# Kernel tuning notes

Hardware: AMD Instinct MI355X
Metric: run time of the kernel (lower is better)

Reference implementation:

```python
import jax, jax.numpy as jnp
import numpy as np


def setup_inputs() -> dict:
    key = jax.random.key(0)
    ks = jax.random.split(key, 6)
    B, N_in, N_out, D_in, D_out, S = 64, 195, 778, 256, 128, 9
    nnz = 3 * N_out
    x = jax.random.normal(ks[0], (B, N_in, D_in), dtype=jnp.float32)
    # upsample transform: each output vertex receives 3 weighted source verts
    row = jnp.repeat(jnp.arange(N_out, dtype=jnp.int64), 3)
    col = jax.random.randint(ks[1], (nnz,), 0, N_in).astype(jnp.int64)
    value = jax.random.uniform(ks[2], (nnz,), dtype=jnp.float32)
    indices = jax.random.randint(ks[3], (N_out, S), 0, N_out).astype(jnp.int64)
    W = jax.random.normal(ks[4], (D_in * S, D_out), dtype=jnp.float32) * 0.02
    b = jnp.zeros((D_out,), dtype=jnp.float32)
    return {"x": x, "row": row, "col": col, "value": value,
            "indices": indices, "W": W, "b": b}


def reference(x, row, col, value, indices, W, b):
    B, N_in, D = x.shape
    N_out, S = indices.shape
    # Pool: gather source verts, scale by barycentric weight, scatter-add
    msg = x[:, col, :] * value[None, :, None]                # (B, nnz, D)
    pooled = jnp.zeros((B, N_out, D), x.dtype).at[:, row, :].add(msg)
    # SpiralConv: gather spiral neighborhood, flatten, linear
    g = pooled[:, indices.reshape(-1), :].reshape(B, N_out, S * D)
    out = jnp.einsum('bnk,ko->bno', g, W) + b                # (B, N_out, D_out)
    return jax.nn.relu(out)
```

## Files before the change

kernel.cpp:

```cpp
#include <hip/hip_runtime.h>
#include <hip/hip_bf16.h>
#include <stdint.h>

#define N_IN 195
#define N_OUT 778
#define D_IN 256
#define D_OUTC 128
#define NS 9
#define KTOT 2304
#define MM 49792
#define BM 256
#define BK 64
#define NWG 195
#define XE 3194880
#define XCVT_BLOCKS 1560
#define POOL_BLOCKS 6224
#define WT_BLOCKS 1152

using short8  = __attribute__((ext_vector_type(8))) short;
using f32x4   = __attribute__((ext_vector_type(4))) float;

__device__ __forceinline__ void gload16(const void* g, void* l) {
  __builtin_amdgcn_global_load_lds(
      (const __attribute__((address_space(1))) uint32_t*)g,
      (__attribute__((address_space(3))) uint32_t*)l, 16, 0, 0);
}

__device__ __forceinline__ unsigned short f2bf(float f) {
  uint32_t u = __float_as_uint(f);
  return (unsigned short)((u + 0x7FFFu + ((u >> 16) & 1u)) >> 16);
}
__device__ __forceinline__ float bf2f(unsigned short s) {
  return __uint_as_float(((uint32_t)s) << 16);
}

__global__ __launch_bounds__(256) void xcvt_kernel(
    const float* __restrict__ x, unsigned short* __restrict__ xh) {
  int i = (blockIdx.x * 256 + threadIdx.x) * 8;
  float4 a = *(const float4*)(x + i);
  float4 b = *(const float4*)(x + i + 4);
  short8 pk;
  pk[0] = (short)f2bf(a.x); pk[1] = (short)f2bf(a.y);
  pk[2] = (short)f2bf(a.z); pk[3] = (short)f2bf(a.w);
  pk[4] = (short)f2bf(b.x); pk[5] = (short)f2bf(b.y);
  pk[6] = (short)f2bf(b.z); pk[7] = (short)f2bf(b.w);
  *(short8*)(xh + i) = pk;
}

__global__ __launch_bounds__(256) void prep_kernel(
    const unsigned short* __restrict__ xh, const int* __restrict__ col,
    const float* __restrict__ value, const float* __restrict__ W,
    unsigned short* __restrict__ pooled, unsigned short* __restrict__ Wt) {
  int bid = blockIdx.x;
  if (bid < POOL_BLOCKS) {
    int m = bid * 8 + (threadIdx.x >> 5);
    int t = threadIdx.x & 31;
    int b = (unsigned)m / N_OUT;
    int n = m - b * N_OUT;
    int j = 3 * n;
    int c0 = col[j], c1 = col[j + 1], c2 = col[j + 2];
    float v0 = value[j], v1 = value[j + 1], v2 = value[j + 2];
    const short8* x0 = (const short8*)(xh + ((size_t)b * N_IN + c0) * D_IN);
    const short8* x1 = (const short8*)(xh + ((size_t)b * N_IN + c1) * D_IN);
    const short8* x2 = (const short8*)(xh + ((size_t)b * N_IN + c2) * D_IN);
    short8 a0 = x0[t], a1 = x1[t], a2 = x2[t];
    short8 pk;
    #pragma unroll
    for (int e = 0; e < 8; ++e) {
      float f = v0 * bf2f((unsigned short)a0[e]) +
                v1 * bf2f((unsigned short)a1[e]) +
                v2 * bf2f((unsigned short)a2[e]);
      pk[e] = (short)f2bf(f);
    }
    ((short8*)(pooled + (size_t)m * D_IN))[t] = pk;
  } else {
    int idx = (bid - POOL_BLOCKS) * 256 + threadIdx.x;
    int o = idx / KTOT, k = idx - o * KTOT;
    Wt[idx] = f2bf(W[(size_t)k * D_OUTC + o]);
  }
}

__global__ __launch_bounds__(512, 2) void gemm_kernel(
    const unsigned short* __restrict__ pooled,
    const unsigned short* __restrict__ Wt,
    const int* __restrict__ indices,
    const float* __restrict__ bias,
    float* __restrict__ out) {
  __shared__ unsigned short Asm[2][BM * BK];
  __shared__ unsigned short Bsm[2][D_OUTC * BK];

  const int tid = threadIdx.x;
  const int wave = tid >> 6, lane = tid & 63;
  const int wr = wave >> 1, wc = wave & 1;

  const int xcd = blockIdx.x & 7, loc = blockIdx.x >> 3;
  const int q8 = NWG >> 3, r8 = NWG & 7;
  const int wg = (xcd < r8 ? xcd * (q8 + 1) : r8 * (q8 + 1) + (xcd - r8) * q8) + loc;
  const int bm = wg * BM;

  const int srow = tid >> 3;
  const int sc = ((tid & 7) ^ (srow & 7)) * 8;
  int nn[4]; size_t gb[4];
  #pragma unroll
  for (int i = 0; i < 4; ++i) {
    int r = i * 64 + srow;
    int m = bm + r; if (m >= MM) m = MM - 1;
    int b = (unsigned)m / N_OUT;
    nn[i] = m - b * N_OUT;
    gb[i] = (size_t)b * N_OUT;
  }
  const unsigned short* wtrow[2];
  #pragma unroll
  for (int i = 0; i < 2; ++i)
    wtrow[i] = Wt + (size_t)(i * 64 + srow) * KTOT + sc;
  char* AsmB = (char*)&Asm[0][0];
  char* BsmB = (char*)&Bsm[0][0];

  int gc[4], gn[4];
  #pragma unroll
  for (int i = 0; i < 4; ++i) gc[i] = indices[nn[i] * NS + 0];

  f32x4 acc[4][4];
  #pragma unroll
  for (int i = 0; i < 4; ++i)
    #pragma unroll
    for (int j = 0; j < 4; ++j) acc[i][j] = f32x4{0.f, 0.f, 0.f, 0.f};

  auto stage = [&](int buf, int s, int q, const int* g) {
    const int kq = s * 256 + q * 64;
    #pragma unroll
    for (int i = 0; i < 4; ++i) {
      const unsigned short* srcA =
          pooled + (((gb[i] + (size_t)g[i]) << 8) + q * 64 + sc);
      gload16(srcA, AsmB + buf * 32768 + i * 8192 + tid * 16);
    }
    #pragma unroll
    for (int i = 0; i < 2; ++i)
      gload16(wtrow[i] + kq, BsmB + buf * 16384 + i * 8192 + tid * 16);
  };

  auto compute = [&](int buf) {
    const char* Ab = AsmB + buf * 32768;
    const char* Bb = BsmB + buf * 16384;
    #pragma unroll
    for (int h = 0; h < 2; ++h) {
      short8 af[4], bf[4];
      const int cb = h * 64 + (lane >> 4) * 16;
      #pragma unroll
      for (int i = 0; i < 4; ++i) {
        int r = wr * 64 + i * 16 + (lane & 15);
        af[i] = *(const short8*)(Ab + r * 128 + (cb ^ ((r & 7) << 4)));
      }
      #pragma unroll
      for (int j = 0; j < 4; ++j) {
        int o = wc * 64 + j * 16 + (lane & 15);
        bf[j] = *(const short8*)(Bb + o * 128 + (cb ^ ((o & 7) << 4)));
      }
      __builtin_amdgcn_s_setprio(1);
      #pragma unroll
      for (int i = 0; i < 4; ++i)
        #pragma unroll
        for (int j = 0; j < 4; ++j)
          acc[i][j] = __builtin_amdgcn_mfma_f32_16x16x32_bf16(
              af[i], bf[j], acc[i][j], 0, 0, 0);
      __builtin_amdgcn_s_setprio(0);
    }
  };

#define WAITV6() asm volatile("s_waitcnt vmcnt(6)" ::: "memory")
#define WAITV0() asm volatile("s_waitcnt vmcnt(0)" ::: "memory")
#define BAR()    __builtin_amdgcn_s_barrier()
#define FENCE()  asm volatile("" ::: "memory")

  stage(0, 0, 0, gc);
  FENCE();

  for (int s = 0; s < NS; ++s) {
    #pragma unroll
    for (int q = 0; q < 4; ++q) {
      const int buf = (s * 4 + q) & 1;
      if (q == 0 && s < NS - 1) {
        #pragma unroll
        for (int i = 0; i < 4; ++i) gn[i] = indices[nn[i] * NS + s + 1];
        FENCE();
      }
      if (q < 3)            stage(buf ^ 1, s, q + 1, gc);
      else if (s < NS - 1)  stage(buf ^ 1, s + 1, 0, gn);
      FENCE();
      if (s == NS - 1 && q == 3) { WAITV0(); } else { WAITV6(); }
      BAR();
      FENCE();
      compute(buf);
      FENCE();
      BAR();
      FENCE();
    }
    #pragma unroll
    for (int i = 0; i < 4; ++i) gc[i] = gn[i];
  }

#undef WAITV6
#undef WAITV0
#undef BAR
#undef FENCE

  #pragma unroll
  for (int j = 0; j < 4; ++j) {
    int colo = wc * 64 + j * 16 + (lane & 15);
    float bo = bias[colo];
    #pragma unroll
    for (int i = 0; i < 4; ++i) {
      int rb = bm + wr * 64 + i * 16 + (lane >> 4) * 4;
      #pragma unroll
      for (int q = 0; q < 4; ++q) {
        int row = rb + q;
        if (row < MM) out[(size_t)row * D_OUTC + colo] = fmaxf(acc[i][j][q] + bo, 0.f);
      }
    }
  }
}

extern "C" void kernel_launch(void* const* d_in, const int* in_sizes, int n_in,
                              void* d_out, int out_size, void* d_ws, size_t ws_size,
                              hipStream_t stream) {
  const float* x       = (const float*)d_in[0];
  const int*   col     = (const int*)d_in[2];
  const float* value   = (const float*)d_in[3];
  const int*   indices = (const int*)d_in[4];
  const float* W       = (const float*)d_in[5];
  const float* bias    = (const float*)d_in[6];
  float* out           = (float*)d_out;

  unsigned short* pooled = (unsigned short*)d_ws;
  unsigned short* Wt  = (unsigned short*)((char*)d_ws + (size_t)MM * D_IN * 2);
  unsigned short* xh  = (unsigned short*)((char*)d_ws + (size_t)MM * D_IN * 2
                                          + (size_t)D_OUTC * KTOT * 2);

  xcvt_kernel<<<XCVT_BLOCKS, 256, 0, stream>>>(x, xh);
  prep_kernel<<<POOL_BLOCKS + WT_BLOCKS, 256, 0, stream>>>(xh, col, value, W,
                                                           pooled, Wt);
  gemm_kernel<<<NWG, 512, 0, stream>>>(pooled, Wt, indices, bias, out);
}
```

Baseline: 71.80 us.

## Use 1024-thread GEMM blocks with triple-buffered LDS prefetch pipeline

The GEMM kernel now launches 1024 threads (16 waves, laid out 4x4) per workgroup instead of 512 (8 waves, 4x2), so each wave owns a 64x32 output tile instead of 64x64. Each thread issues fewer staging loads. LDS buffering goes from double to triple, with prefetch two stages ahead and adjusted vmcnt waits plus a peeled tail. The aim is more latency hiding for the gathered loads and more waves in flight. In exchange, each wave reuses the A fragments across fewer MFMAs, LDS use rises to 144KB, and occupancy is capped at one block per CU.

```diff
diff --git a/kernel.cpp b/kernel.cpp
--- a/kernel.cpp
+++ b/kernel.cpp
@@ -80,18 +80,18 @@
   }
 }
 
-__global__ __launch_bounds__(512, 2) void gemm_kernel(
+__global__ __launch_bounds__(1024, 1) void gemm_kernel(
     const unsigned short* __restrict__ pooled,
     const unsigned short* __restrict__ Wt,
     const int* __restrict__ indices,
     const float* __restrict__ bias,
     float* __restrict__ out) {
-  __shared__ unsigned short Asm[2][BM * BK];
-  __shared__ unsigned short Bsm[2][D_OUTC * BK];
+  __shared__ unsigned short Asm[3][BM * BK];
+  __shared__ unsigned short Bsm[3][D_OUTC * BK];
 
   const int tid = threadIdx.x;
   const int wave = tid >> 6, lane = tid & 63;
-  const int wr = wave >> 1, wc = wave & 1;
+  const int wr = wave >> 2, wc = wave & 3;
 
   const int xcd = blockIdx.x & 7, loc = blockIdx.x >> 3;
   const int q8 = NWG >> 3, r8 = NWG & 7;
@@ -100,43 +100,38 @@
 
   const int srow = tid >> 3;
   const int sc = ((tid & 7) ^ (srow & 7)) * 8;
-  int nn[4]; size_t gb[4];
-  #pragma unroll
-  for (int i = 0; i < 4; ++i) {
-    int r = i * 64 + srow;
+  int nn[2]; size_t gb[2];
+  #pragma unroll
+  for (int i = 0; i < 2; ++i) {
+    int r = i * 128 + srow;
     int m = bm + r; if (m >= MM) m = MM - 1;
     int b = (unsigned)m / N_OUT;
     nn[i] = m - b * N_OUT;
     gb[i] = (size_t)b * N_OUT;
   }
-  const unsigned short* wtrow[2];
-  #pragma unroll
-  for (int i = 0; i < 2; ++i)
-    wtrow[i] = Wt + (size_t)(i * 64 + srow) * KTOT + sc;
+  const unsigned short* wtrow = Wt + (size_t)srow * KTOT + sc;
   char* AsmB = (char*)&Asm[0][0];
   char* BsmB = (char*)&Bsm[0][0];
 
-  int gc[4], gn[4];
-  #pragma unroll
-  for (int i = 0; i < 4; ++i) gc[i] = indices[nn[i] * NS + 0];
-
-  f32x4 acc[4][4];
+  int gc[2], gn[2];
+  #pragma unroll
+  for (int i = 0; i < 2; ++i) gc[i] = indices[nn[i] * NS + 0];
+
+  f32x4 acc[4][2];
   #pragma unroll
   for (int i = 0; i < 4; ++i)
     #pragma unroll
-    for (int j = 0; j < 4; ++j) acc[i][j] = f32x4{0.f, 0.f, 0.f, 0.f};
+    for (int j = 0; j < 2; ++j) acc[i][j] = f32x4{0.f, 0.f, 0.f, 0.f};
 
   auto stage = [&](int buf, int s, int q, const int* g) {
     const int kq = s * 256 + q * 64;
     #pragma unroll
-    for (int i = 0; i < 4; ++i) {
+    for (int i = 0; i < 2; ++i) {
       const unsigned short* srcA =
           pooled + (((gb[i] + (size_t)g[i]) << 8) + q * 64 + sc);
-      gload16(srcA, AsmB + buf * 32768 + i * 8192 + tid * 16);
-    }
-    #pragma unroll
-    for (int i = 0; i < 2; ++i)
-      gload16(wtrow[i] + kq, BsmB + buf * 16384 + i * 8192 + tid * 16);
+      gload16(srcA, AsmB + buf * 32768 + i * 16384 + tid * 16);
+    }
+    gload16(wtrow + kq, BsmB + buf * 16384 + tid * 16);
   };
 
   auto compute = [&](int buf) {
@@ -144,7 +139,7 @@
     const char* Bb = BsmB + buf * 16384;
     #pragma unroll
     for (int h = 0; h < 2; ++h) {
-      short8 af[4], bf[4];
+      short8 af[4], bf[2];
       const int cb = h * 64 + (lane >> 4) * 16;
       #pragma unroll
       for (int i = 0; i < 4; ++i) {
@@ -152,61 +147,82 @@
         af[i] = *(const short8*)(Ab + r * 128 + (cb ^ ((r & 7) << 4)));
       }
       #pragma unroll
-      for (int j = 0; j < 4; ++j) {
-        int o = wc * 64 + j * 16 + (lane & 15);
+      for (int j = 0; j < 2; ++j) {
+        int o = wc * 32 + j * 16 + (lane & 15);
         bf[j] = *(const short8*)(Bb + o * 128 + (cb ^ ((o & 7) << 4)));
       }
       __builtin_amdgcn_s_setprio(1);
       #pragma unroll
       for (int i = 0; i < 4; ++i)
         #pragma unroll
-        for (int j = 0; j < 4; ++j)
+        for (int j = 0; j < 2; ++j)
           acc[i][j] = __builtin_amdgcn_mfma_f32_16x16x32_bf16(
               af[i], bf[j], acc[i][j], 0, 0, 0);
       __builtin_amdgcn_s_setprio(0);
     }
   };
 
+#define WAITV8() asm volatile("s_waitcnt vmcnt(8)" ::: "memory")
 #define WAITV6() asm volatile("s_waitcnt vmcnt(6)" ::: "memory")
+#define WAITV3() asm volatile("s_waitcnt vmcnt(3)" ::: "memory")
 #define WAITV0() asm volatile("s_waitcnt vmcnt(0)" ::: "memory")
 #define BAR()    __builtin_amdgcn_s_barrier()
 #define FENCE()  asm volatile("" ::: "memory")
 
-  stage(0, 0, 0, gc);
-  FENCE();
-
-  for (int s = 0; s < NS; ++s) {
+  stage(0, 0, 0, gc); FENCE();
+  stage(1, 0, 1, gc); FENCE();
+
+  int bc = 0;
+  for (int s = 0; s < 8; ++s) {
     #pragma unroll
     for (int q = 0; q < 4; ++q) {
-      const int buf = (s * 4 + q) & 1;
-      if (q == 0 && s < NS - 1) {
+      const int bs = bc == 0 ? 2 : bc - 1;
+      if (q < 2) stage(bs, s, q + 2, gc);
+      else       stage(bs, s + 1, q - 2, gn);
+      FENCE();
+      if (q == 0) {
         #pragma unroll
-        for (int i = 0; i < 4; ++i) gn[i] = indices[nn[i] * NS + s + 1];
+        for (int i = 0; i < 2; ++i) gn[i] = indices[nn[i] * NS + s + 1];
         FENCE();
-      }
-      if (q < 3)            stage(buf ^ 1, s, q + 1, gc);
-      else if (s < NS - 1)  stage(buf ^ 1, s + 1, 0, gn);
-      FENCE();
-      if (s == NS - 1 && q == 3) { WAITV0(); } else { WAITV6(); }
-      BAR();
-      FENCE();
-      compute(buf);
-      FENCE();
-      BAR();
-      FENCE();
-    }
-    #pragma unroll
-    for (int i = 0; i < 4; ++i) gc[i] = gn[i];
-  }
-
+        WAITV8();
+      } else {
+        WAITV6();
+      }
+      BAR(); FENCE();
+      compute(bc);
+      FENCE(); BAR();
+      bc = bc == 2 ? 0 : bc + 1;
+    }
+    #pragma unroll
+    for (int i = 0; i < 2; ++i) gc[i] = gn[i];
+  }
+  {
+    int bs = bc == 0 ? 2 : bc - 1;
+    stage(bs, 8, 2, gc); FENCE();
+    WAITV6(); BAR(); FENCE(); compute(bc); FENCE(); BAR();
+    bc = bc == 2 ? 0 : bc + 1;
+
+    bs = bc == 0 ? 2 : bc - 1;
+    stage(bs, 8, 3, gc); FENCE();
+    WAITV6(); BAR(); FENCE(); compute(bc); FENCE(); BAR();
+    bc = bc == 2 ? 0 : bc + 1;
+
+    WAITV3(); BAR(); FENCE(); compute(bc); FENCE(); BAR();
+    bc = bc == 2 ? 0 : bc + 1;
+
+    WAITV0(); BAR(); FENCE(); compute(bc); FENCE(); BAR();
+  }
+
+#undef WAITV8
 #undef WAITV6
+#undef WAITV3
 #undef WAITV0
 #undef BAR
 #undef FENCE
 
   #pragma unroll
-  for (int j = 0; j < 4; ++j) {
-    int colo = wc * 64 + j * 16 + (lane & 15);
+  for (int j = 0; j < 2; ++j) {
+    int colo = wc * 32 + j * 16 + (lane & 15);
     float bo = bias[colo];
     #pragma unroll
     for (int i = 0; i < 4; ++i) {
@@ -239,5 +255,5 @@
   xcvt_kernel<<<XCVT_BLOCKS, 256, 0, stream>>>(x, xh);
   prep_kernel<<<POOL_BLOCKS + WT_BLOCKS, 256, 0, stream>>>(xh, col, value, W,
                                                            pooled, Wt);
-  gemm_kernel<<<NWG, 512, 0, stream>>>(pooled, Wt, indices, bias, out);
-}
+  gemm_kernel<<<NWG, 1024, 0, stream>>>(pooled, Wt, indices, bias, out);
+}
```

Measured after the change: 69.40 us. 1.03x faster.
